# Kernel optimization log

Measured on AMD Instinct MI355X. Metric: run time of the kernel, lower is better.

Reference implementation:

```python
import jax, jax.numpy as jnp
import numpy as np

N, D, S = 262144, 512, 8192
EPS = 0.006  # constant offset added in the original module


def setup_inputs() -> dict:
    key = jax.random.key(0)
    k1, k2 = jax.random.split(key)
    x = jax.random.normal(k1, (N, D), dtype=jnp.float32)
    # Build S contiguous, non-overlapping inclusive [start, end] boundaries
    cuts = jnp.sort(jax.random.randint(k2, (S - 1,), 1, N, dtype=jnp.int32))
    starts = jnp.concatenate([jnp.zeros((1,), jnp.int32), cuts])
    ends = jnp.concatenate([cuts, jnp.full((1,), N, jnp.int32)]) - 1
    ends = jnp.maximum(ends, starts)  # guard against empty segments
    graph = jnp.stack([starts, ends], axis=1)  # [S, 2] int32
    return {"input": x, "graph": graph}


def reference(input, graph):
    # Per-segment mean over rows start..end (inclusive), + 0.006.
    # Single-pass vectorized form via an exclusive prefix sum:
    #   sum(input[s:e+1]) = P[e+1] - P[s]
    P = jnp.concatenate(
        [jnp.zeros((1, input.shape[1]), input.dtype), jnp.cumsum(input, axis=0)],
        axis=0,
    )  # [N+1, D]
    starts = graph[:, 0]
    ends = graph[:, 1]
    seg_sum = P[ends + 1] - P[starts]  # [S, D]
    counts = (ends - starts + 1).astype(input.dtype)
    return seg_sum / counts[:, None] + jnp.asarray(EPS, input.dtype)
```

## Files before the change

### kernel.cpp

```cpp
#include <hip/hip_runtime.h>


#define EPS_VAL 0.006f
#define DIM 512
#define DV 128
#define TILE 32
#define GROUP 4
#define NGROUPS (TILE / GROUP)

__global__ __launch_bounds__(256) void zero_out_kernel(float4* __restrict__ out, int n4) {
  int i = blockIdx.x * 256 + threadIdx.x;
  if (i < n4) out[i] = make_float4(0.f, 0.f, 0.f, 0.f);
}

__global__ __launch_bounds__(128) void pool_tile_kernel(
    const float* __restrict__ x,
    const int* __restrict__ graph,
    float* __restrict__ out,
    int N, int S) {
  const int r0 = blockIdx.x * TILE;
  const int r1 = r0 + TILE - 1;
  const int t = threadIdx.x;

  int lo = 0, hi = S - 1;
  while (lo < hi) {
    int mid = (lo + hi) >> 1;
    if (graph[2 * mid + 1] < r0) lo = mid + 1; else hi = mid;
  }

  int s = lo;
  int seg_st = graph[2 * s];
  int seg_en = graph[2 * s + 1];
  int nx_st = (s + 1 < S) ? graph[2 * s + 2] : N;
  int nx_en = (s + 1 < S) ? graph[2 * s + 3] : N;

  const float4* xp = reinterpret_cast<const float4*>(x) + (size_t)r0 * DV + t;

  float4 acc = make_float4(0.f, 0.f, 0.f, 0.f);
  float4 buf[GROUP];
#pragma unroll
  for (int j = 0; j < GROUP; ++j) buf[j] = xp[j * DV];
  xp += GROUP * DV;

#pragma unroll
  for (int g = 0; g < NGROUPS; ++g) {
    float4 nbuf[GROUP];
    if (g + 1 < NGROUPS) {
#pragma unroll
      for (int j = 0; j < GROUP; ++j) nbuf[j] = xp[j * DV];
      xp += GROUP * DV;
    }
#pragma unroll
    for (int j = 0; j < GROUP; ++j) {
      const int r = r0 + g * GROUP + j;
      const float4 v = buf[j];
      acc.x += v.x; acc.y += v.y; acc.z += v.z; acc.w += v.w;
      while (r == seg_en) {
        const float inv = 1.0f / (float)(seg_en - seg_st + 1);
        float4 res;
        res.x = acc.x * inv; res.y = acc.y * inv;
        res.z = acc.z * inv; res.w = acc.w * inv;
        float* op = out + (size_t)s * DIM + t * 4;
        if (seg_st >= r0) {
          res.x += EPS_VAL; res.y += EPS_VAL; res.z += EPS_VAL; res.w += EPS_VAL;
          *reinterpret_cast<float4*>(op) = res;
        } else {
          unsafeAtomicAdd(op + 0, res.x);
          unsafeAtomicAdd(op + 1, res.y);
          unsafeAtomicAdd(op + 2, res.z);
          unsafeAtomicAdd(op + 3, res.w);
        }
        ++s;
        seg_st = nx_st; seg_en = nx_en;
        if (s + 1 < S) {
          nx_st = graph[2 * s + 2];
          nx_en = graph[2 * s + 3];
        } else {
          nx_st = N; nx_en = N;
        }
        if (seg_st <= r) { acc = v; } else { acc = make_float4(0.f, 0.f, 0.f, 0.f); }
      }
    }
#pragma unroll
    for (int j = 0; j < GROUP; ++j) buf[j] = nbuf[j];
  }

  if (s < S && seg_st <= r1) {
    const float inv = 1.0f / (float)(seg_en - seg_st + 1);
    float4 res;
    res.x = acc.x * inv; res.y = acc.y * inv;
    res.z = acc.z * inv; res.w = acc.w * inv;
    if (seg_st >= r0) {
      res.x += EPS_VAL; res.y += EPS_VAL; res.z += EPS_VAL; res.w += EPS_VAL;
    }
    float* op = out + (size_t)s * DIM + t * 4;
    unsafeAtomicAdd(op + 0, res.x);
    unsafeAtomicAdd(op + 1, res.y);
    unsafeAtomicAdd(op + 2, res.z);
    unsafeAtomicAdd(op + 3, res.w);
  }
}

extern "C" void kernel_launch(void* const* d_in, const int* in_sizes, int n_in,
                              void* d_out, int out_size, void* d_ws, size_t ws_size,
                              hipStream_t stream) {
  const float* x = (const float*)d_in[0];
  const int* graph = (const int*)d_in[1];
  float* out = (float*)d_out;

  const int N = in_sizes[0] / DIM;
  const int S = in_sizes[1] / 2;

  const int n4 = out_size / 4;
  zero_out_kernel<<<(n4 + 255) / 256, 256, 0, stream>>>(
      reinterpret_cast<float4*>(out), n4);

  const int ntiles = N / TILE;
  pool_tile_kernel<<<ntiles, 128, 0, stream>>>(x, graph, out, N, S);
}
```

Measured before the change: 129.6 us.

## Precompute tile segment lookup, stage descriptors in LDS, use nontemporal loads

Moves the per-tile binary search over segment ends into the init kernel that also zeroes the output, storing each tile's starting segment index in workspace. The pool kernel then stages up to 16 segment descriptors in shared memory instead of issuing dependent global reads of the graph. Input rows are read with nontemporal loads, the prefetch group grows from 4 to 8 rows, and the float4 arithmetic is written with vector types. This adds a __syncthreads and a workspace dependency, and the larger prefetch group raises register use.

```diff
diff --git a/kernel.cpp b/kernel.cpp
--- a/kernel.cpp
+++ b/kernel.cpp
@@ -5,65 +5,80 @@
 #define DIM 512
 #define DV 128
 #define TILE 32
-#define GROUP 4
+#define GROUP 8
 #define NGROUPS (TILE / GROUP)
+#define MAXSEG 16
 
-__global__ __launch_bounds__(256) void zero_out_kernel(float4* __restrict__ out, int n4) {
-  int i = blockIdx.x * 256 + threadIdx.x;
-  if (i < n4) out[i] = make_float4(0.f, 0.f, 0.f, 0.f);
+typedef float f32x4 __attribute__((ext_vector_type(4)));
+
+__global__ __launch_bounds__(256) void init_kernel(
+    f32x4* __restrict__ out, int n4,
+    const int* __restrict__ graph, int* __restrict__ lo_arr,
+    int ntiles, int S) {
+  const int i = blockIdx.x * 256 + threadIdx.x;
+  if (i < n4) out[i] = (f32x4){0.f, 0.f, 0.f, 0.f};
+  if (i < ntiles) {
+    const int r0 = i * TILE;
+    int lo = 0, hi = S - 1;
+    while (lo < hi) {
+      int mid = (lo + hi) >> 1;
+      if (graph[2 * mid + 1] < r0) lo = mid + 1; else hi = mid;
+    }
+    lo_arr[i] = lo;
+  }
 }
 
 __global__ __launch_bounds__(128) void pool_tile_kernel(
     const float* __restrict__ x,
     const int* __restrict__ graph,
+    const int* __restrict__ lo_arr,
     float* __restrict__ out,
     int N, int S) {
+  __shared__ int2 sdesc[MAXSEG];
   const int r0 = blockIdx.x * TILE;
   const int r1 = r0 + TILE - 1;
   const int t = threadIdx.x;
 
-  int lo = 0, hi = S - 1;
-  while (lo < hi) {
-    int mid = (lo + hi) >> 1;
-    if (graph[2 * mid + 1] < r0) lo = mid + 1; else hi = mid;
+  const int lo = lo_arr[blockIdx.x];
+  if (t < MAXSEG) {
+    const int si = lo + t;
+    sdesc[t] = (si < S) ? reinterpret_cast<const int2*>(graph)[si]
+                        : make_int2(N, N);
   }
+  __syncthreads();
 
   int s = lo;
-  int seg_st = graph[2 * s];
-  int seg_en = graph[2 * s + 1];
-  int nx_st = (s + 1 < S) ? graph[2 * s + 2] : N;
-  int nx_en = (s + 1 < S) ? graph[2 * s + 3] : N;
+  int seg_st = sdesc[0].x;
+  int seg_en = sdesc[0].y;
 
-  const float4* xp = reinterpret_cast<const float4*>(x) + (size_t)r0 * DV + t;
+  const f32x4* xp = reinterpret_cast<const f32x4*>(x) + (size_t)r0 * DV + t;
 
-  float4 acc = make_float4(0.f, 0.f, 0.f, 0.f);
-  float4 buf[GROUP];
+  f32x4 acc = (f32x4){0.f, 0.f, 0.f, 0.f};
+  f32x4 buf[GROUP];
 #pragma unroll
-  for (int j = 0; j < GROUP; ++j) buf[j] = xp[j * DV];
+  for (int j = 0; j < GROUP; ++j) buf[j] = __builtin_nontemporal_load(xp + j * DV);
   xp += GROUP * DV;
 
 #pragma unroll
   for (int g = 0; g < NGROUPS; ++g) {
-    float4 nbuf[GROUP];
+    f32x4 nbuf[GROUP];
     if (g + 1 < NGROUPS) {
 #pragma unroll
-      for (int j = 0; j < GROUP; ++j) nbuf[j] = xp[j * DV];
+      for (int j = 0; j < GROUP; ++j) nbuf[j] = __builtin_nontemporal_load(xp + j * DV);
       xp += GROUP * DV;
     }
 #pragma unroll
     for (int j = 0; j < GROUP; ++j) {
       const int r = r0 + g * GROUP + j;
-      const float4 v = buf[j];
-      acc.x += v.x; acc.y += v.y; acc.z += v.z; acc.w += v.w;
+      const f32x4 v = buf[j];
+      acc += v;
       while (r == seg_en) {
         const float inv = 1.0f / (float)(seg_en - seg_st + 1);
-        float4 res;
-        res.x = acc.x * inv; res.y = acc.y * inv;
-        res.z = acc.z * inv; res.w = acc.w * inv;
+        f32x4 res = acc * inv;
         float* op = out + (size_t)s * DIM + t * 4;
         if (seg_st >= r0) {
-          res.x += EPS_VAL; res.y += EPS_VAL; res.z += EPS_VAL; res.w += EPS_VAL;
-          *reinterpret_cast<float4*>(op) = res;
+          res += EPS_VAL;
+          *reinterpret_cast<f32x4*>(op) = res;
         } else {
           unsafeAtomicAdd(op + 0, res.x);
           unsafeAtomicAdd(op + 1, res.y);
@@ -71,14 +86,17 @@
           unsafeAtomicAdd(op + 3, res.w);
         }
         ++s;
-        seg_st = nx_st; seg_en = nx_en;
-        if (s + 1 < S) {
-          nx_st = graph[2 * s + 2];
-          nx_en = graph[2 * s + 3];
+        const int widx = s - lo;
+        int2 nx;
+        if (widx < MAXSEG) {
+          nx = sdesc[widx];
         } else {
-          nx_st = N; nx_en = N;
+          nx = (s < S) ? reinterpret_cast<const int2*>(graph)[s]
+                       : make_int2(N, N);
         }
-        if (seg_st <= r) { acc = v; } else { acc = make_float4(0.f, 0.f, 0.f, 0.f); }
+        seg_st = nx.x; seg_en = nx.y;
+        if (seg_st <= r) { acc = v; }
+        else { acc = (f32x4){0.f, 0.f, 0.f, 0.f}; }
       }
     }
 #pragma unroll
@@ -87,11 +105,9 @@
 
   if (s < S && seg_st <= r1) {
     const float inv = 1.0f / (float)(seg_en - seg_st + 1);
-    float4 res;
-    res.x = acc.x * inv; res.y = acc.y * inv;
-    res.z = acc.z * inv; res.w = acc.w * inv;
+    f32x4 res = acc * inv;
     if (seg_st >= r0) {
-      res.x += EPS_VAL; res.y += EPS_VAL; res.z += EPS_VAL; res.w += EPS_VAL;
+      res += EPS_VAL;
     }
     float* op = out + (size_t)s * DIM + t * 4;
     unsafeAtomicAdd(op + 0, res.x);
@@ -107,14 +123,16 @@
   const float* x = (const float*)d_in[0];
   const int* graph = (const int*)d_in[1];
   float* out = (float*)d_out;
+  int* lo_arr = (int*)d_ws;
 
   const int N = in_sizes[0] / DIM;
   const int S = in_sizes[1] / 2;
+  const int ntiles = N / TILE;
+  const int n4 = out_size / 4;
 
-  const int n4 = out_size / 4;
-  zero_out_kernel<<<(n4 + 255) / 256, 256, 0, stream>>>(
-      reinterpret_cast<float4*>(out), n4);
+  const int init_items = (n4 > ntiles) ? n4 : ntiles;
+  init_kernel<<<(init_items + 255) / 256, 256, 0, stream>>>(
+      reinterpret_cast<f32x4*>(out), n4, graph, lo_arr, ntiles, S);
 
-  const int ntiles = N / TILE;
-  pool_tile_kernel<<<ntiles, 128, 0, stream>>>(x, graph, out, N, S);
+  pool_tile_kernel<<<ntiles, 128, 0, stream>>>(x, graph, lo_arr, out, N, S);
 }
```

New measurement: 123.1 us. 5.0% less time.
